# Performance work log

Measured on AMD Instinct MI355X. Metric: run time of the kernel, lower is better.

## Reference

```python
import jax, jax.numpy as jnp
import numpy as np

NA = 50000; NB = 50000
F = 128; H = 256; O = 16
E = 1000000; L = 100000
NEG_SLOPE = 0.2


def _gat_conv(xs, xd, ei, W, a_s, a_d, b, n_dst):
    # Bipartite PyG GATConv (heads=1, add_self_loops=False):
    # shared linear on src/dst, LeakyReLU attention logits, segment softmax
    # over destination nodes, scatter-weighted-sum aggregation + bias.
    hs = xs @ W            # [Ns, Fout]
    hd = xd @ W            # [Nd, Fout]
    src, dst = ei[0], ei[1]
    logit = (hs * a_s).sum(-1)[src] + (hd * a_d).sum(-1)[dst]   # [E]
    logit = jnp.where(logit > 0, logit, NEG_SLOPE * logit)      # leaky_relu
    m = jax.ops.segment_max(logit, dst, num_segments=n_dst)
    m = jnp.where(jnp.isfinite(m), m, 0.0)                      # empty segments
    ex = jnp.exp(logit - m[dst])
    den = jax.ops.segment_sum(ex, dst, num_segments=n_dst)
    alpha = ex / (den[dst] + 1e-16)
    out = jax.ops.segment_sum(hs[src] * alpha[:, None], dst, num_segments=n_dst)
    return out + b


def setup_inputs() -> dict:
    key = jax.random.key(0)
    ks = jax.random.split(key, 40)
    d = {}
    d["x_A"] = jax.random.normal(ks[0], (NA, F), jnp.float32)
    d["x_B"] = jax.random.normal(ks[1], (NB, F), jnp.float32)
    d["ei_ab"] = jax.random.randint(ks[2], (2, E), 0, NB)
    d["ei_ba"] = jax.random.randint(ks[3], (2, E), 0, NA)
    d["src_idx"] = jax.random.randint(ks[4], (L,), 0, NA)
    d["dst_idx"] = jax.random.randint(ks[5], (L,), 0, NB)
    dims = [(F, H), (H, H), (H, O)]
    i = 6
    for l, (fi, fo) in enumerate(dims, 1):
        for t in ("ab", "ba"):
            d["W%d%s" % (l, t)] = jax.random.normal(ks[i], (fi, fo), jnp.float32) / np.float32(np.sqrt(fi)); i += 1
            d["as%d%s" % (l, t)] = jax.random.normal(ks[i], (fo,), jnp.float32) * 0.1; i += 1
            d["ad%d%s" % (l, t)] = jax.random.normal(ks[i], (fo,), jnp.float32) * 0.1; i += 1
            d["b%d%s" % (l, t)] = jnp.zeros((fo,), jnp.float32)
    return d


def reference(x_A, x_B, ei_ab, ei_ba, src_idx, dst_idx,
              W1ab, as1ab, ad1ab, b1ab, W1ba, as1ba, ad1ba, b1ba,
              W2ab, as2ab, ad2ab, b2ab, W2ba, as2ba, ad2ba, b2ba,
              W3ab, as3ab, ad3ab, b3ab, W3ba, as3ba, ad3ba, b3ba):
    p_ab = [(W1ab, as1ab, ad1ab, b1ab), (W2ab, as2ab, ad2ab, b2ab), (W3ab, as3ab, ad3ab, b3ab)]
    p_ba = [(W1ba, as1ba, ad1ba, b1ba), (W2ba, as2ba, ad2ba, b2ba), (W3ba, as3ba, ad3ba, b3ba)]
    xa, xb = x_A, x_B
    for l in range(3):
        W, a_s, a_d, b = p_ab[l]
        nb = _gat_conv(xa, xb, ei_ab, W, a_s, a_d, b, NB)
        W, a_s, a_d, b = p_ba[l]
        na = _gat_conv(xb, xa, ei_ba, W, a_s, a_d, b, NA)
        if l < 2:
            xa, xb = jax.nn.relu(na), jax.nn.relu(nb)
        else:
            xa, xb = na, nb
    # (emb_A[src] @ emb_B[dst].T).sum(-1) == emb_A[src] @ emb_B[dst].sum(0)
    pred = xa[src_idx] @ xb[dst_idx].sum(axis=0)
    return pred, xa, xb
```

## Files before the change

kernel.cpp:

```cpp
#include <hip/hip_runtime.h>
#include <hip/hip_bf16.h>

#define WAVE 64

typedef __attribute__((ext_vector_type(8))) short short8;
typedef __attribute__((ext_vector_type(8))) unsigned short ushort8_t;
typedef __attribute__((ext_vector_type(4))) float f32x4;

__device__ __forceinline__ unsigned short f32_to_bf16_rne(float f) {
    unsigned int u = __float_as_uint(f);
    u = u + 0x7fffu + ((u >> 16) & 1u);
    return (unsigned short)(u >> 16);
}
__device__ __forceinline__ float bf16_to_f32(unsigned short h) {
    return __uint_as_float((unsigned int)h << 16);
}

__global__ void hist_kernel(const int* __restrict__ dst, int E, int* __restrict__ cnt) {
    int e = blockIdx.x * blockDim.x + threadIdx.x;
    if (e < E) atomicAdd(&cnt[dst[e]], 1);
}

__global__ __launch_bounds__(1024) void exscan_kernel(const int* __restrict__ cnt,
                                                      int* __restrict__ off, int N) {
    __shared__ int part[1024];
    int t = threadIdx.x;
    int chunk = (N + 1023) / 1024;
    int lo = t * chunk;
    int hi = lo + chunk; if (hi > N) hi = N;
    int s = 0;
    for (int i = lo; i < hi; ++i) s += cnt[i];
    part[t] = s;
    __syncthreads();
    for (int o = 1; o < 1024; o <<= 1) {
        int v = (t >= o) ? part[t - o] : 0;
        __syncthreads();
        part[t] += v;
        __syncthreads();
    }
    int run = (t == 0) ? 0 : part[t - 1];
    for (int i = lo; i < hi; ++i) { off[i] = run; run += cnt[i]; }
    if (t == 1023) off[N] = part[1023];
}

__global__ void fill_kernel(const int* __restrict__ src, const int* __restrict__ dst, int E,
                            const int* __restrict__ off, int* __restrict__ cursor,
                            int* __restrict__ csr_src) {
    int e = blockIdx.x * blockDim.x + threadIdx.x;
    if (e < E) {
        int d = dst[e];
        int pos = off[d] + atomicAdd(&cursor[d], 1);
        csr_src[pos] = src[e];
    }
}

__global__ void cvt_bf16_kernel(const float* __restrict__ in, unsigned short* __restrict__ out,
                                int n4) {
    int i = blockIdx.x * blockDim.x + threadIdx.x;
    if (i >= n4) return;
    float4 v = *(const float4*)(in + (size_t)i * 4);
    ushort4 o;
    o.x = f32_to_bf16_rne(v.x);
    o.y = f32_to_bf16_rne(v.y);
    o.z = f32_to_bf16_rne(v.z);
    o.w = f32_to_bf16_rne(v.w);
    *(ushort4*)(out + (size_t)i * 4) = o;
}

__global__ void wt_bf16_kernel(const float* __restrict__ W, unsigned short* __restrict__ WT,
                               int K, int N) {
    int idx = blockIdx.x * blockDim.x + threadIdx.x;
    if (idx >= K * N) return;
    int k = idx / N, n = idx - k * N;
    WT[(size_t)n * K + k] = f32_to_bf16_rne(W[idx]);
}

__global__ void rowdot_kernel(const float* __restrict__ X, const float* __restrict__ v,
                              float* __restrict__ out, int N, int F) {
    int w = (blockIdx.x * blockDim.x + threadIdx.x) >> 6;
    int lane = threadIdx.x & 63;
    if (w >= N) return;
    const float* row = X + (size_t)w * F;
    float s = 0.f;
    for (int f = lane; f < F; f += WAVE) s += row[f] * v[f];
    #pragma unroll
    for (int o = 32; o; o >>= 1) s += __shfl_xor(s, o);
    if (lane == 0) out[w] = s;
}

__global__ void rowdot_bf16(const unsigned short* __restrict__ X, const float* __restrict__ v,
                            float* __restrict__ out, int N, int F) {
    int w = (blockIdx.x * blockDim.x + threadIdx.x) >> 6;
    int lane = threadIdx.x & 63;
    if (w >= N) return;
    const unsigned short* row = X + (size_t)w * F;
    float s = 0.f;
    for (int f = lane << 2; f < F; f += 256) {
        ushort4 hv = *(const ushort4*)(row + f);
        s += bf16_to_f32(hv.x) * v[f + 0] + bf16_to_f32(hv.y) * v[f + 1]
           + bf16_to_f32(hv.z) * v[f + 2] + bf16_to_f32(hv.w) * v[f + 3];
    }
    #pragma unroll
    for (int o = 32; o; o >>= 1) s += __shfl_xor(s, o);
    if (lane == 0) out[w] = s;
}

#define GBM 128
#define GBN 64
#define GBK 64
#define LDP (GBK + 8)

__global__ __launch_bounds__(256) void gemm_bf16(const unsigned short* __restrict__ A,
                                                 const unsigned short* __restrict__ BT,
                                                 unsigned short* __restrict__ C,
                                                 int M, int N, int K) {
    __shared__ unsigned short As[GBM][LDP];
    __shared__ unsigned short Bs[GBN][LDP];

    int tid  = threadIdx.x;
    int lane = tid & 63;
    int wid  = tid >> 6;
    int wr   = wid >> 1;
    int wc   = wid & 1;
    int ln   = lane & 15;
    int hi   = lane >> 4;

    int row0 = blockIdx.x * GBM;
    int col0 = blockIdx.y * GBN;

    int sr = tid >> 3;
    int sk = (tid & 7) << 3;

    f32x4 acc[4][2];
    #pragma unroll
    for (int i = 0; i < 4; ++i)
        #pragma unroll
        for (int j = 0; j < 2; ++j)
            acc[i][j] = (f32x4){0.f, 0.f, 0.f, 0.f};

    for (int k0 = 0; k0 < K; k0 += GBK) {
        #pragma unroll
        for (int p = 0; p < 4; ++p) {
            int r = sr + p * 32;
            int gr = row0 + r;
            short8 v = (short8){0,0,0,0,0,0,0,0};
            if (gr < M)
                v = *(const short8*)(A + (size_t)gr * K + k0 + sk);
            *(short8*)&As[r][sk] = v;
        }
        #pragma unroll
        for (int p = 0; p < 2; ++p) {
            int r = sr + p * 32;
            short8 v = *(const short8*)(BT + (size_t)(col0 + r) * K + k0 + sk);
            *(short8*)&Bs[r][sk] = v;
        }
        __syncthreads();

        #pragma unroll
        for (int kk = 0; kk < 2; ++kk) {
            short8 a[4], b[2];
            #pragma unroll
            for (int mi = 0; mi < 4; ++mi)
                a[mi] = *(const short8*)&As[wr * 64 + mi * 16 + ln][kk * 32 + hi * 8];
            #pragma unroll
            for (int ni = 0; ni < 2; ++ni)
                b[ni] = *(const short8*)&Bs[wc * 32 + ni * 16 + ln][kk * 32 + hi * 8];
            #pragma unroll
            for (int mi = 0; mi < 4; ++mi)
                #pragma unroll
                for (int ni = 0; ni < 2; ++ni)
                    acc[mi][ni] = __builtin_amdgcn_mfma_f32_16x16x32_bf16(
                        a[mi], b[ni], acc[mi][ni], 0, 0, 0);
        }
        __syncthreads();
    }

    #pragma unroll
    for (int mi = 0; mi < 4; ++mi) {
        #pragma unroll
        for (int ni = 0; ni < 2; ++ni) {
            int gcol = col0 + wc * 32 + ni * 16 + ln;
            #pragma unroll
            for (int r = 0; r < 4; ++r) {
                int grow = row0 + wr * 64 + mi * 16 + hi * 4 + r;
                if (grow < M) C[(size_t)grow * N + gcol] = f32_to_bf16_rne(acc[mi][ni][r]);
            }
        }
    }
}

__global__ __launch_bounds__(256) void gemm_bf16_n16(const unsigned short* __restrict__ A,
                                                     const float* __restrict__ B,
                                                     float* __restrict__ C, int M) {
    __shared__ float Bs[4096];
    for (int t = threadIdx.x; t < 4096; t += 256) Bs[t] = B[t];
    __syncthreads();
    int w = (blockIdx.x * blockDim.x + threadIdx.x) >> 6;
    int lane = threadIdx.x & 63;
    if (w >= M) return;
    int n = lane & 15, kg = lane >> 4;
    const unsigned short* row = A + (size_t)w * 256 + kg * 64;
    const float* Bp = Bs + kg * 64 * 16 + n;
    float s = 0.f;
    #pragma unroll
    for (int j = 0; j < 64; j += 4) {
        ushort4 a4 = *(const ushort4*)(row + j);
        s += bf16_to_f32(a4.x) * Bp[(j + 0) * 16]
           + bf16_to_f32(a4.y) * Bp[(j + 1) * 16]
           + bf16_to_f32(a4.z) * Bp[(j + 2) * 16]
           + bf16_to_f32(a4.w) * Bp[(j + 3) * 16];
    }
    s += __shfl_xor(s, 16);
    s += __shfl_xor(s, 32);
    if (lane < 16) C[(size_t)w * 16 + n] = s;
}

template <bool RELU>
__global__ __launch_bounds__(256) void gat_agg256(
        const unsigned short* __restrict__ H, const float* __restrict__ ssrc,
        const float* __restrict__ sdst, const int* __restrict__ off,
        const int* __restrict__ csr, const float* __restrict__ bias,
        unsigned short* __restrict__ out, int Nd) {
    int wid = (blockIdx.x * blockDim.x + threadIdx.x) >> 6;
    int lane = threadIdx.x & 63;
    if (wid >= Nd) return;
    int s0 = off[wid], s1 = off[wid + 1];
    float sd = sdst[wid];

    float mx = -1e30f;
    for (int i = s0 + lane; i < s1; i += WAVE) {
        float l = ssrc[csr[i]] + sd;
        l = (l > 0.f) ? l : 0.2f * l;
        mx = fmaxf(mx, l);
    }
    #pragma unroll
    for (int o = 32; o; o >>= 1) mx = fmaxf(mx, __shfl_xor(mx, o));
    float m = (s1 > s0) ? mx : 0.f;

    int h = lane >> 5;
    int fo = (lane & 31) << 3;
    float den = 0.f;
    float acc[8] = {0.f, 0.f, 0.f, 0.f, 0.f, 0.f, 0.f, 0.f};
    for (int chunk = s0; chunk < s1; chunk += WAVE) {
        int i = chunk + lane;
        int si = 0; float w = 0.f;
        if (i < s1) {
            si = csr[i];
            float l = ssrc[si] + sd;
            l = (l > 0.f) ? l : 0.2f * l;
            w = __expf(l - m);
        }
        den += w;
        int cnt = min(WAVE, s1 - chunk);
        int iters = (cnt + 1) >> 1;
        for (int it = 0; it < iters; ++it) {
            int j = (it << 1) + h;
            int jc = (j < cnt) ? j : 0;
            float wj = __shfl(w, jc);
            int sj = __shfl(si, jc);
            if (j < cnt) {
                ushort8_t hv = *(const ushort8_t*)(H + (size_t)sj * 256 + fo);
                #pragma unroll
                for (int t = 0; t < 8; ++t)
                    acc[t] += wj * bf16_to_f32(hv[t]);
            }
        }
    }
    #pragma unroll
    for (int o = 32; o; o >>= 1) den += __shfl_xor(den, o);
    float inv = 1.f / (den + 1e-16f);
    #pragma unroll
    for (int t = 0; t < 8; ++t) acc[t] += __shfl_xor(acc[t], 32);

    if (h == 0) {
        float bv[8];
        *(float4*)&bv[0] = *(const float4*)(bias + fo);
        *(float4*)&bv[4] = *(const float4*)(bias + fo + 4);
        ushort8_t ov;
        #pragma unroll
        for (int t = 0; t < 8; ++t) {
            float v = acc[t] * inv + bv[t];
            if (RELU) v = fmaxf(v, 0.f);
            ov[t] = f32_to_bf16_rne(v);
        }
        *(ushort8_t*)(out + (size_t)wid * 256 + fo) = ov;
    }
}

__global__ __launch_bounds__(256) void gat_agg16(
        const float* __restrict__ H, const float* __restrict__ ssrc,
        const float* __restrict__ sdst, const int* __restrict__ off,
        const int* __restrict__ csr, const float* __restrict__ bias,
        float* __restrict__ out, int Nd) {
    int wid = (blockIdx.x * blockDim.x + threadIdx.x) >> 6;
    int lane = threadIdx.x & 63;
    if (wid >= Nd) return;
    int s0 = off[wid], s1 = off[wid + 1];
    float sd = sdst[wid];

    float mx = -1e30f;
    for (int i = s0 + lane; i < s1; i += WAVE) {
        float l = ssrc[csr[i]] + sd;
        l = (l > 0.f) ? l : 0.2f * l;
        mx = fmaxf(mx, l);
    }
    #pragma unroll
    for (int o = 32; o; o >>= 1) mx = fmaxf(mx, __shfl_xor(mx, o));
    float m = (s1 > s0) ? mx : 0.f;

    float den = 0.f;
    float acc = 0.f;
    int eg = lane >> 4, n = lane & 15;
    for (int chunk = s0; chunk < s1; chunk += WAVE) {
        int i = chunk + lane;
        int si = 0; float w = 0.f;
        if (i < s1) {
            si = csr[i];
            float l = ssrc[si] + sd;
            l = (l > 0.f) ? l : 0.2f * l;
            w = __expf(l - m);
        }
        den += w;
        int cnt = min(WAVE, s1 - chunk);
        for (int j0 = 0; j0 < cnt; j0 += 4) {
            int jj = j0 + eg;
            float wj = __shfl(w, jj & 63);
            int sj = __shfl(si, jj & 63);
            if (jj < cnt) acc += wj * H[(size_t)sj * 16 + n];
        }
    }
    #pragma unroll
    for (int o = 32; o; o >>= 1) den += __shfl_xor(den, o);
    float inv = 1.f / (den + 1e-16f);
    acc += __shfl_xor(acc, 16);
    acc += __shfl_xor(acc, 32);
    if (lane < 16)
        out[(size_t)wid * 16 + n] = acc * inv + bias[n];
}

__global__ void sum_rows16(const float* __restrict__ X, const int* __restrict__ idx,
                           int L, float* __restrict__ accum) {
    __shared__ float red[16][16];
    int f = threadIdx.x & 15, r = threadIdx.x >> 4;
    float acc = 0.f;
    for (int i = blockIdx.x * 16 + r; i < L; i += gridDim.x * 16)
        acc += X[(size_t)idx[i] * 16 + f];
    red[r][f] = acc;
    __syncthreads();
    #pragma unroll
    for (int o = 8; o; o >>= 1) {
        if (r < o) red[r][f] += red[r + o][f];
        __syncthreads();
    }
    if (r == 0) atomicAdd(&accum[f], red[0][f]);
}

__global__ void pred16(const float* __restrict__ XA, const int* __restrict__ sidx,
                       const float* __restrict__ accum, float* __restrict__ pred, int L) {
    int i = blockIdx.x * blockDim.x + threadIdx.x;
    if (i >= L) return;
    const float* row = XA + (size_t)sidx[i] * 16;
    float s = 0.f;
    #pragma unroll
    for (int f = 0; f < 16; ++f) s += row[f] * accum[f];
    pred[i] = s;
}

extern "C" void kernel_launch(void* const* d_in, const int* in_sizes, int n_in,
                              void* d_out, int out_size, void* d_ws, size_t ws_size,
                              hipStream_t stream) {
    const float* xA = (const float*)d_in[0];
    const float* xB = (const float*)d_in[1];
    const int* ei_ab = (const int*)d_in[2];
    const int* ei_ba = (const int*)d_in[3];
    const int* src_idx = (const int*)d_in[4];
    const int* dst_idx = (const int*)d_in[5];

    const int NAn = in_sizes[0] / 128;
    const int NBn = in_sizes[1] / 128;
    const int E   = in_sizes[2] / 2;
    const int L   = in_sizes[4];

    const float* Wab[3]  = {(const float*)d_in[6],  (const float*)d_in[14], (const float*)d_in[22]};
    const float* asab[3] = {(const float*)d_in[7],  (const float*)d_in[15], (const float*)d_in[23]};
    const float* adab[3] = {(const float*)d_in[8],  (const float*)d_in[16], (const float*)d_in[24]};
    const float* bab[3]  = {(const float*)d_in[9],  (const float*)d_in[17], (const float*)d_in[25]};
    const float* Wba[3]  = {(const float*)d_in[10], (const float*)d_in[18], (const float*)d_in[26]};
    const float* asba[3] = {(const float*)d_in[11], (const float*)d_in[19], (const float*)d_in[27]};
    const float* adba[3] = {(const float*)d_in[12], (const float*)d_in[20], (const float*)d_in[28]};
    const float* bba[3]  = {(const float*)d_in[13], (const float*)d_in[21], (const float*)d_in[29]};

    float* outp   = (float*)d_out;
    float* pred   = outp;
    float* xa_out = outp + L;
    float* xb_out = outp + L + (size_t)NAn * 16;

    char* p = (char*)d_ws;
    auto alloc = [&](size_t n) { char* r = p; p += (n + 255) & ~(size_t)255; return r; };
    unsigned short* FA0 = (unsigned short*)alloc((size_t)NAn * 256 * 2);
    unsigned short* FB0 = (unsigned short*)alloc((size_t)NBn * 256 * 2);
    unsigned short* FA1 = (unsigned short*)alloc((size_t)NAn * 256 * 2);
    unsigned short* FB1 = (unsigned short*)alloc((size_t)NBn * 256 * 2);
    unsigned short* Hb16 = (unsigned short*)alloc((size_t)NAn * 256 * 2);
    unsigned short* WT  = (unsigned short*)alloc((size_t)256 * 256 * 2);
    float* ssrc = (float*)alloc((size_t)NAn * 4);
    float* sdst = (float*)alloc((size_t)NAn * 4);
    float* wv   = (float*)alloc(256 * 4);
    int* csr_ab = (int*)alloc((size_t)E * 4);
    int* csr_ba = (int*)alloc((size_t)E * 4);
    int* off_ab = (int*)alloc((size_t)(NBn + 1) * 4);
    int* off_ba = (int*)alloc((size_t)(NAn + 1) * 4);
    int* cnt_ab = (int*)alloc((size_t)NBn * 4);
    int* cur_ab = (int*)alloc((size_t)NBn * 4);
    int* cnt_ba = (int*)alloc((size_t)NAn * 4);
    int* cur_ba = (int*)alloc((size_t)NAn * 4);
    float* accum16 = (float*)alloc(16 * 4);
    if ((size_t)(p - (char*)d_ws) > ws_size) return;

    hipMemsetAsync(cnt_ab, 0, (size_t)NBn * 4, stream);
    hipMemsetAsync(cur_ab, 0, (size_t)NBn * 4, stream);
    hipMemsetAsync(cnt_ba, 0, (size_t)NAn * 4, stream);
    hipMemsetAsync(cur_ba, 0, (size_t)NAn * 4, stream);
    int eb = (E + 255) / 256;
    hist_kernel<<<eb, 256, 0, stream>>>(ei_ab + E, E, cnt_ab);
    exscan_kernel<<<1, 1024, 0, stream>>>(cnt_ab, off_ab, NBn);
    fill_kernel<<<eb, 256, 0, stream>>>(ei_ab, ei_ab + E, E, off_ab, cur_ab, csr_ab);
    hist_kernel<<<eb, 256, 0, stream>>>(ei_ba + E, E, cnt_ba);
    exscan_kernel<<<1, 1024, 0, stream>>>(cnt_ba, off_ba, NAn);
    fill_kernel<<<eb, 256, 0, stream>>>(ei_ba, ei_ba + E, E, off_ba, cur_ba, csr_ba);

    cvt_bf16_kernel<<<(NAn * 128 / 4 + 255) / 256, 256, 0, stream>>>(xA, FA0, NAn * 128 / 4);
    cvt_bf16_kernel<<<(NBn * 128 / 4 + 255) / 256, 256, 0, stream>>>(xB, FB0, NBn * 128 / 4);

    auto conv256 = [&](const unsigned short* xs, const unsigned short* xd,
                       int Ns, int Nd, int Fin,
                       const float* W, const float* a_s, const float* a_d,
                       const float* bias, const int* off, const int* csr,
                       unsigned short* out, bool relu) {
        wt_bf16_kernel<<<(Fin * 256 + 255) / 256, 256, 0, stream>>>(W, WT, Fin, 256);
        dim3 gg((Ns + GBM - 1) / GBM, 256 / GBN);
        gemm_bf16<<<gg, 256, 0, stream>>>(xs, WT, Hb16, Ns, 256, Fin);
        rowdot_bf16<<<(Ns * 64 + 255) / 256, 256, 0, stream>>>(Hb16, a_s, ssrc, Ns, 256);
        rowdot_kernel<<<(Fin * 64 + 255) / 256, 256, 0, stream>>>(W, a_d, wv, Fin, 256);
        rowdot_bf16<<<(Nd * 64 + 255) / 256, 256, 0, stream>>>(xd, wv, sdst, Nd, Fin);
        int ab = (Nd + 3) / 4;
        if (relu)
            gat_agg256<true><<<ab, 256, 0, stream>>>(Hb16, ssrc, sdst, off, csr, bias, out, Nd);
        else
            gat_agg256<false><<<ab, 256, 0, stream>>>(Hb16, ssrc, sdst, off, csr, bias, out, Nd);
    };

    auto conv16 = [&](const unsigned short* xs, const unsigned short* xd,
                      int Ns, int Nd,
                      const float* W, const float* a_s, const float* a_d,
                      const float* bias, const int* off, const int* csr,
                      float* out) {
        float* Hb32 = (float*)Hb16;
        gemm_bf16_n16<<<(Ns + 3) / 4, 256, 0, stream>>>(xs, W, Hb32, Ns);
        rowdot_kernel<<<(Ns * 64 + 255) / 256, 256, 0, stream>>>(Hb32, a_s, ssrc, Ns, 16);
        rowdot_kernel<<<(256 * 64 + 255) / 256, 256, 0, stream>>>(W, a_d, wv, 256, 16);
        rowdot_bf16<<<(Nd * 64 + 255) / 256, 256, 0, stream>>>(xd, wv, sdst, Nd, 256);
        gat_agg16<<<(Nd + 3) / 4, 256, 0, stream>>>(Hb32, ssrc, sdst, off, csr, bias, out, Nd);
    };

    conv256(FA0, FB0, NAn, NBn, 128, Wab[0], asab[0], adab[0], bab[0], off_ab, csr_ab, FB1, true);
    conv256(FB0, FA0, NBn, NAn, 128, Wba[0], asba[0], adba[0], bba[0], off_ba, csr_ba, FA1, true);
    conv256(FA1, FB1, NAn, NBn, 256, Wab[1], asab[1], adab[1], bab[1], off_ab, csr_ab, FB0, true);
    conv256(FB1, FA1, NBn, NAn, 256, Wba[1], asba[1], adba[1], bba[1], off_ba, csr_ba, FA0, true);
    conv16(FA0, FB0, NAn, NBn, Wab[2], asab[2], adab[2], bab[2], off_ab, csr_ab, xb_out);
    conv16(FB0, FA0, NBn, NAn, Wba[2], asba[2], adba[2], bba[2], off_ba, csr_ba, xa_out);

    hipMemsetAsync(accum16, 0, 16 * 4, stream);
    sum_rows16<<<128, 256, 0, stream>>>(xb_out, dst_idx, L, accum16);
    pred16<<<(L + 255) / 256, 256, 0, stream>>>(xa_out, src_idx, accum16, pred, L);
}
```

Measured before the change: 1.177 ms.

## Replace single-block serial exclusive scan with three-phase multi-block scan

The CSR offset scan previously ran in one 1024-thread block, with each thread serially walking about 49 counts using strided, uncoalesced reads. It is now split into three kernels: per-256 chunk reduction, a single-block scan of the ~196 chunk sums, and a per-chunk block scan that adds the chunk base. This spreads the scan across many CUs with coalesced accesses, at the cost of two extra kernel launches per edge type.

```diff
diff --git a/kernel.cpp b/kernel.cpp
--- a/kernel.cpp
+++ b/kernel.cpp
@@ -21,16 +21,27 @@
     if (e < E) atomicAdd(&cnt[dst[e]], 1);
 }
 
-__global__ __launch_bounds__(1024) void exscan_kernel(const int* __restrict__ cnt,
-                                                      int* __restrict__ off, int N) {
+__global__ __launch_bounds__(256) void chunk_sum_kernel(const int* __restrict__ cnt,
+                                                        int* __restrict__ csum, int N) {
+    __shared__ int red[256];
+    int t = threadIdx.x;
+    int i = blockIdx.x * 256 + t;
+    red[t] = (i < N) ? cnt[i] : 0;
+    __syncthreads();
+    #pragma unroll
+    for (int o = 128; o; o >>= 1) {
+        if (t < o) red[t] += red[t + o];
+        __syncthreads();
+    }
+    if (t == 0) csum[blockIdx.x] = red[0];
+}
+
+__global__ __launch_bounds__(1024) void exscan_sums_kernel(const int* __restrict__ csum,
+                                                           int* __restrict__ cbase, int C,
+                                                           int* __restrict__ totalOut) {
     __shared__ int part[1024];
     int t = threadIdx.x;
-    int chunk = (N + 1023) / 1024;
-    int lo = t * chunk;
-    int hi = lo + chunk; if (hi > N) hi = N;
-    int s = 0;
-    for (int i = lo; i < hi; ++i) s += cnt[i];
-    part[t] = s;
+    part[t] = (t < C) ? csum[t] : 0;
     __syncthreads();
     for (int o = 1; o < 1024; o <<= 1) {
         int v = (t >= o) ? part[t - o] : 0;
@@ -38,9 +49,25 @@
         part[t] += v;
         __syncthreads();
     }
-    int run = (t == 0) ? 0 : part[t - 1];
-    for (int i = lo; i < hi; ++i) { off[i] = run; run += cnt[i]; }
-    if (t == 1023) off[N] = part[1023];
+    if (t < C) cbase[t] = (t == 0) ? 0 : part[t - 1];
+    if (t == 1023) *totalOut = part[1023];
+}
+
+__global__ __launch_bounds__(256) void chunk_scan_kernel(const int* __restrict__ cnt,
+                                                         const int* __restrict__ cbase,
+                                                         int* __restrict__ off, int N) {
+    __shared__ int s[256];
+    int t = threadIdx.x;
+    int i = blockIdx.x * 256 + t;
+    s[t] = (i < N) ? cnt[i] : 0;
+    __syncthreads();
+    for (int o = 1; o < 256; o <<= 1) {
+        int v = (t >= o) ? s[t - o] : 0;
+        __syncthreads();
+        s[t] += v;
+        __syncthreads();
+    }
+    if (i < N) off[i] = cbase[blockIdx.x] + ((t == 0) ? 0 : s[t - 1]);
 }
 
 __global__ void fill_kernel(const int* __restrict__ src, const int* __restrict__ dst, int E,
@@ -414,6 +441,8 @@
     int* cur_ab = (int*)alloc((size_t)NBn * 4);
     int* cnt_ba = (int*)alloc((size_t)NAn * 4);
     int* cur_ba = (int*)alloc((size_t)NAn * 4);
+    int* csum   = (int*)alloc(1024 * 4);
+    int* cbase  = (int*)alloc(1024 * 4);
     float* accum16 = (float*)alloc(16 * 4);
     if ((size_t)(p - (char*)d_ws) > ws_size) return;
 
@@ -422,11 +451,17 @@
     hipMemsetAsync(cnt_ba, 0, (size_t)NAn * 4, stream);
     hipMemsetAsync(cur_ba, 0, (size_t)NAn * 4, stream);
     int eb = (E + 255) / 256;
+    int Cab = (NBn + 255) / 256;
+    int Cba = (NAn + 255) / 256;
     hist_kernel<<<eb, 256, 0, stream>>>(ei_ab + E, E, cnt_ab);
-    exscan_kernel<<<1, 1024, 0, stream>>>(cnt_ab, off_ab, NBn);
+    chunk_sum_kernel<<<Cab, 256, 0, stream>>>(cnt_ab, csum, NBn);
+    exscan_sums_kernel<<<1, 1024, 0, stream>>>(csum, cbase, Cab, off_ab + NBn);
+    chunk_scan_kernel<<<Cab, 256, 0, stream>>>(cnt_ab, cbase, off_ab, NBn);
     fill_kernel<<<eb, 256, 0, stream>>>(ei_ab, ei_ab + E, E, off_ab, cur_ab, csr_ab);
     hist_kernel<<<eb, 256, 0, stream>>>(ei_ba + E, E, cnt_ba);
-    exscan_kernel<<<1, 1024, 0, stream>>>(cnt_ba, off_ba, NAn);
+    chunk_sum_kernel<<<Cba, 256, 0, stream>>>(cnt_ba, csum, NAn);
+    exscan_sums_kernel<<<1, 1024, 0, stream>>>(csum, cbase, Cba, off_ba + NAn);
+    chunk_scan_kernel<<<Cba, 256, 0, stream>>>(cnt_ba, cbase, off_ba, NAn);
     fill_kernel<<<eb, 256, 0, stream>>>(ei_ba, ei_ba + E, E, off_ba, cur_ba, csr_ba);
 
     cvt_bf16_kernel<<<(NAn * 128 / 4 + 255) / 256, 256, 0, stream>>>(xA, FA0, NAn * 128 / 4);
```

After: 1.042 ms. -11.5%, faster.
